# Kernel tuning notes

Hardware: AMD Instinct MI355X
Metric: run time of the kernel (lower is better)

The kernel has to match this reference:

```python
import jax, jax.numpy as jnp
import numpy as np

NUM_SEQS = 4
Q_LEN = 512          # new query tokens per sequence (chunked prefill)
SEQ_LEN = 2048       # total tokens per sequence (context + query)
NUM_Q_HEADS = 32
NUM_KV_HEADS = 8
HEAD_SIZE = 128
BLOCK_SIZE = 32
BLOCKS_PER_SEQ = SEQ_LEN // BLOCK_SIZE          # 64
NUM_BLOCKS = NUM_SEQS * BLOCKS_PER_SEQ          # 256 physical blocks


def setup_inputs() -> dict:
    key = jax.random.key(0)
    k1, k2, k3 = jax.random.split(key, 3)
    query = jax.random.normal(k1, (NUM_SEQS * Q_LEN, NUM_Q_HEADS, HEAD_SIZE), dtype=jnp.float32)
    key_cache = jax.random.normal(k2, (NUM_BLOCKS, BLOCK_SIZE, NUM_KV_HEADS, HEAD_SIZE), dtype=jnp.float32)
    value_cache = jax.random.normal(k3, (NUM_BLOCKS, BLOCK_SIZE, NUM_KV_HEADS, HEAD_SIZE), dtype=jnp.float32)
    # each sequence owns a contiguous run of physical blocks (any permutation works)
    block_tables = jnp.arange(NUM_BLOCKS, dtype=jnp.int32).reshape(NUM_SEQS, BLOCKS_PER_SEQ)
    seq_lens = jnp.full((NUM_SEQS,), SEQ_LEN, dtype=jnp.int32)
    query_start_loc = jnp.arange(NUM_SEQS + 1, dtype=jnp.int32) * Q_LEN
    return {"query": query, "key_cache": key_cache, "value_cache": value_cache,
            "block_tables": block_tables, "seq_lens": seq_lens,
            "query_start_loc": query_start_loc}


def reference(query, key_cache, value_cache, block_tables, seq_lens, query_start_loc):
    # paged/unified attention, base config: causal, GQA, no window/alibi/softcap/sinks/quant
    B, NB = block_tables.shape
    BS = key_cache.shape[1]
    total_q, Hq, D = query.shape
    Kvh = key_cache.shape[2]
    G = Hq // Kvh                       # num_queries_per_kv
    Lq = total_q // B                   # uniform query len per seq (matches query_start_loc)
    S = NB * BS                         # max kv length covered by block table
    scale = D ** -0.5

    q = query.reshape(B, Lq, Kvh, G, D)
    # gather paged KV: [B, NB, BS, Kvh, D] -> [B, S, Kvh, D]
    k = key_cache[block_tables].reshape(B, S, Kvh, D)
    v = value_cache[block_tables].reshape(B, S, Kvh, D)

    scores = jnp.einsum('blkgd,bskd->blkgs', q, k) * scale  # [B, Lq, Kvh, G, S]

    # absolute query positions: context_len + local pos, context_len = seq_len - Lq
    q_abs = (seq_lens - Lq)[:, None] + jnp.arange(Lq, dtype=seq_lens.dtype)[None, :]  # [B, Lq]
    kpos = jnp.arange(S, dtype=seq_lens.dtype)
    causal = kpos[None, None, :] <= q_abs[:, :, None]                 # key <= query pos
    valid = kpos[None, None, :] < seq_lens[:, None, None]             # key within seq
    mask = causal & valid                                             # [B, Lq, S]

    neg_inf = jnp.asarray(-jnp.inf, scores.dtype)
    scores = jnp.where(mask[:, :, None, None, :], scores, neg_inf)
    p = jax.nn.softmax(scores, axis=-1)
    out = jnp.einsum('blkgs,bskd->blkgd', p, v)                       # [B, Lq, Kvh, G, D]
    return out.reshape(total_q, Hq, D)
```

## Files before the change

kernel.cpp:

```cpp
#include <hip/hip_runtime.h>
#include <hip/hip_bf16.h>

typedef __bf16 bf16;
typedef __attribute__((ext_vector_type(8))) __bf16 bf16x8;
typedef __attribute__((ext_vector_type(4))) __bf16 bf16x4;
typedef __attribute__((ext_vector_type(4))) float f32x4;

static constexpr int NSEQ = 4;
static constexpr int LQ   = 512;
static constexpr int HQN  = 32;
static constexpr int HKVN = 8;
static constexpr int GQ   = 4;
static constexpr int DH   = 128;
static constexpr int BPS  = 64;
static constexpr int SKV  = 2048;
static constexpr int KVB  = 64;
static constexpr int QBL  = 32;
static constexpr int VST  = 72;

__device__ __forceinline__ bf16x8 cvt8(const float4& a, const float4& b) {
  bf16x8 o;
  o[0] = (bf16)a.x; o[1] = (bf16)a.y; o[2] = (bf16)a.z; o[3] = (bf16)a.w;
  o[4] = (bf16)b.x; o[5] = (bf16)b.y; o[6] = (bf16)b.z; o[7] = (bf16)b.w;
  return o;
}

__global__ void prep_k(const float* __restrict__ kc, const int* __restrict__ bt,
                       bf16* __restrict__ kb) {
  int e = (blockIdx.x * 256 + threadIdx.x) * 8;
  int d = e & 127;
  int s = (e >> 7) & 2047;
  int h = (e >> 18) & 7;
  int b = e >> 21;
  int pb = bt[b * BPS + (s >> 5)];
  const float* src = kc + (((size_t)pb * 32 + (s & 31)) * 8 + h) * 128 + d;
  float4 a = *(const float4*)src;
  float4 c = *(const float4*)(src + 4);
  *(bf16x8*)(kb + e) = cvt8(a, c);
}

__global__ void prep_vt(const float* __restrict__ vc, const int* __restrict__ bt,
                        bf16* __restrict__ vt) {
  __shared__ __align__(16) bf16 T[64][136];
  int bid = blockIdx.x;
  int st = bid & 31;
  int h  = (bid >> 5) & 7;
  int b  = bid >> 8;
  int tid = threadIdx.x;
  {
    int s  = tid >> 2;
    int d0 = (tid & 3) * 32;
    int sg = st * 64 + s;
    int pb = bt[b * BPS + (sg >> 5)];
    const float* src = vc + (((size_t)pb * 32 + (sg & 31)) * 8 + h) * 128 + d0;
#pragma unroll
    for (int k = 0; k < 4; ++k) {
      float4 a = *(const float4*)(src + 8 * k);
      float4 c = *(const float4*)(src + 8 * k + 4);
      *(bf16x8*)&T[s][d0 + 8 * k] = cvt8(a, c);
    }
  }
  __syncthreads();
  {
    int d  = tid & 127;
    int g2 = tid >> 7;
    bf16* dst = vt + (((size_t)(b * 8 + h)) * 128 + d) * SKV + st * 64 + g2 * 32;
#pragma unroll
    for (int k = 0; k < 4; ++k) {
      bf16x8 o;
#pragma unroll
      for (int j = 0; j < 8; ++j) o[j] = T[g2 * 32 + k * 8 + j][d];
      *(bf16x8*)(dst + 8 * k) = o;
    }
  }
}

template <bool WS>
__global__ __launch_bounds__(256, 2)
void attn_kern(const float* __restrict__ q, const float* __restrict__ kc,
               const float* __restrict__ vc, const int* __restrict__ bt,
               const int* __restrict__ seq_lens, const bf16* __restrict__ kb,
               const bf16* __restrict__ vtb, float* __restrict__ out) {
  __shared__ __align__(16) bf16 Kl[2][64][136];
  __shared__ __align__(16) bf16 Vl[2][128 * VST];

  int bid = (int)blockIdx.x;
  int hi  = bid >> 8;
  int u   = bid & 255;
  int xcd = u & 7;
  int k2  = u >> 3;
  int c   = (k2 >> 3) | (xcd << 2);
  int i   = k2 & 7;
  int qt  = hi ? (15 - i) : i;
  int h   = c & 7;
  int b   = c >> 3;
  int lb  = qt * QBL;

  int tid  = (int)threadIdx.x;
  int w    = tid >> 6;
  int lane = tid & 63;
  int lq   = lane & 15;
  int lg   = lane >> 4;

  int ctx = seq_lens[b] - LQ;
  int nt  = (ctx + lb + QBL + KVB - 1) / KVB;

  const float CEXP = 0.08838834764831843f * 1.44269504088896340f;
  const float TH8  = 8.0f / CEXP;

  int hq = h * GQ + w;
  bf16x8 qf[2][4];
#pragma unroll
  for (int n = 0; n < 2; ++n) {
    const float* qp = q + (((size_t)(b * LQ + lb + n * 16 + lq)) * HQN + hq) * DH + lg * 8;
#pragma unroll
    for (int kk = 0; kk < 4; ++kk) {
      float4 a = *(const float4*)(qp + kk * 32);
      float4 c2 = *(const float4*)(qp + kk * 32 + 4);
      qf[n][kk] = cvt8(a, c2);
    }
  }

  f32x4 accO[2][8];
  f32x4 zero = {0.f, 0.f, 0.f, 0.f};
#pragma unroll
  for (int m = 0; m < 2; ++m)
#pragma unroll
    for (int nd = 0; nd < 8; ++nd) accO[m][nd] = zero;
  float mrun[2] = {-1e30f, -1e30f};
  float lrun[2] = {0.f, 0.f};

  const int* btr = bt + b * BPS;
  const bf16* kbase = WS ? kb  + (size_t)(b * 8 + h) * SKV * DH : nullptr;
  const bf16* vbase = WS ? vtb + (size_t)(b * 8 + h) * DH * SKV : nullptr;

  int ks_ = tid >> 2, kd0 = (tid & 3) * 32;
  int vd_ = tid >> 1, vu  = tid & 1;
  int vxw = ((vd_ >> 3) & 3) << 1;

  bf16x8 kpre[4], vpre[4];
  auto ldKV = [&](int t) {
    const bf16* ks = kbase + ((size_t)t * 64 + ks_) * DH + kd0;
#pragma unroll
    for (int k = 0; k < 4; ++k) kpre[k] = *(const bf16x8*)(ks + 8 * k);
    const bf16* vs = vbase + (size_t)vd_ * SKV + t * 64 + vu * 32;
#pragma unroll
    for (int k = 0; k < 4; ++k) vpre[k] = *(const bf16x8*)(vs + 8 * k);
  };
  auto stKV = [&](int bb) {
#pragma unroll
    for (int k = 0; k < 4; ++k) *(bf16x8*)&Kl[bb][ks_][kd0 + 8 * k] = kpre[k];
#pragma unroll
    for (int k = 0; k < 4; ++k) {
      int g = (4 * vu + k) ^ vxw;
      *(bf16x8*)&Vl[bb][vd_ * VST + (g << 3)] = vpre[k];
    }
  };

  auto compute = [&](int t, int bb) {
    f32x4 accS[4][2];
#pragma unroll
    for (int m = 0; m < 4; ++m)
#pragma unroll
      for (int n = 0; n < 2; ++n) accS[m][n] = zero;
    __builtin_amdgcn_s_setprio(1);
#pragma unroll
    for (int m = 0; m < 4; ++m) {
      bf16x8 ak[4];
#pragma unroll
      for (int kk = 0; kk < 4; ++kk)
        ak[kk] = *(const bf16x8*)&Kl[bb][m * 16 + lq][kk * 32 + lg * 8];
#pragma unroll
      for (int n = 0; n < 2; ++n)
#pragma unroll
        for (int kk = 0; kk < 4; ++kk)
          accS[m][n] = __builtin_amdgcn_mfma_f32_16x16x32_bf16(ak[kk], qf[n][kk], accS[m][n], 0, 0, 0);
    }
    __builtin_amdgcn_s_setprio(0);

    if (t * KVB + KVB - 1 > ctx + lb) {
#pragma unroll
      for (int m = 0; m < 4; ++m) {
        int sg = t * 64 + m * 16 + lg * 4;
#pragma unroll
        for (int n = 0; n < 2; ++n) {
          int qpos = ctx + lb + n * 16 + lq;
#pragma unroll
          for (int r = 0; r < 4; ++r)
            if (sg + r > qpos) accS[m][n][r] = -1e30f;
        }
      }
    }

#pragma unroll
    for (int n = 0; n < 2; ++n) {
      float mx = accS[0][n][0];
#pragma unroll
      for (int m = 0; m < 4; ++m)
#pragma unroll
        for (int r = 0; r < 4; ++r) mx = fmaxf(mx, accS[m][n][r]);
      mx = fmaxf(mx, __shfl_xor(mx, 16));
      mx = fmaxf(mx, __shfl_xor(mx, 32));
      if (!__all(mx <= mrun[n] + TH8)) {
        float mnew = fmaxf(mrun[n], mx);
        float corr = exp2f((mrun[n] - mnew) * CEXP);
        mrun[n] = mnew;
        lrun[n] *= corr;
        float cb[4];
#pragma unroll
        for (int r = 0; r < 4; ++r) cb[r] = __shfl(corr, lg * 4 + r);
#pragma unroll
        for (int nd = 0; nd < 8; ++nd)
#pragma unroll
          for (int r = 0; r < 4; ++r) accO[n][nd][r] *= cb[r];
      }
      float psum = 0.f;
#pragma unroll
      for (int m = 0; m < 4; ++m)
#pragma unroll
        for (int r = 0; r < 4; ++r) {
          float p = exp2f((accS[m][n][r] - mrun[n]) * CEXP);
          psum += p;
          accS[m][n][r] = p;
        }
      lrun[n] += psum;
    }

    bf16x8 ap[2][2];
#pragma unroll
    for (int n = 0; n < 2; ++n)
#pragma unroll
      for (int ks3 = 0; ks3 < 2; ++ks3) {
#pragma unroll
        for (int e = 0; e < 4; ++e) {
          ap[n][ks3][e]     = (bf16)accS[2 * ks3][n][e];
          ap[n][ks3][4 + e] = (bf16)accS[2 * ks3 + 1][n][e];
        }
      }

    __builtin_amdgcn_s_setprio(1);
#pragma unroll
    for (int nd = 0; nd < 8; ++nd) {
      int d   = nd * 16 + lq;
      int vxr = ((d >> 3) & 3) << 1;
      int rb  = d * VST + 4 * (lg & 1);
#pragma unroll
      for (int ks3 = 0; ks3 < 2; ++ks3) {
        int g0 = 4 * ks3 + (lg >> 1);
        bf16x4 lo = *(const bf16x4*)&Vl[bb][rb + ((g0 ^ vxr) << 3)];
        bf16x4 hi2 = *(const bf16x4*)&Vl[bb][rb + (((g0 + 2) ^ vxr) << 3)];
        bf16x8 bv;
#pragma unroll
        for (int e = 0; e < 4; ++e) { bv[e] = lo[e]; bv[4 + e] = hi2[e]; }
#pragma unroll
        for (int n = 0; n < 2; ++n)
          accO[n][nd] = __builtin_amdgcn_mfma_f32_16x16x32_bf16(ap[n][ks3], bv, accO[n][nd], 0, 0, 0);
      }
    }
    __builtin_amdgcn_s_setprio(0);
  };

  if (WS) {
    ldKV(0);
    stKV(0);
    if (nt > 1) ldKV(1);
    __syncthreads();
    for (int t = 0; t < nt; ++t) {
      int cur = t & 1;
      if (t + 1 < nt) {
        stKV(cur ^ 1);
        if (t + 2 < nt) ldKV(t + 2);
      }
      compute(t, cur);
      __syncthreads();
    }
  } else {
    for (int t = 0; t < nt; ++t) {
      {
        int s  = tid >> 2;
        int d0 = (tid & 3) * 32;
        int pb = btr[t * 2 + (s >> 5)];
        const float* ksrc = kc + (((size_t)pb * 32 + (s & 31)) * 8 + h) * 128 + d0;
#pragma unroll
        for (int k = 0; k < 4; ++k) {
          float4 a = *(const float4*)(ksrc + 8 * k);
          float4 c2 = *(const float4*)(ksrc + 8 * k + 4);
          *(bf16x8*)&Kl[0][s][d0 + 8 * k] = cvt8(a, c2);
        }
        int d  = tid & 127;
        int sh = tid >> 7;
        int vxf = ((d >> 3) & 3) << 1;
        int pbv = btr[t * 2 + sh];
        const float* vsrc = vc + (((size_t)pbv * 32) * 8 + h) * 128 + d;
#pragma unroll
        for (int k = 0; k < 8; ++k) {
          bf16x4 o;
#pragma unroll
          for (int j = 0; j < 4; ++j) o[j] = (bf16)vsrc[(size_t)(k * 4 + j) * 1024];
          int g = (4 * sh + (k >> 1)) ^ vxf;
          *(bf16x4*)&Vl[0][d * VST + (g << 3) + 4 * (k & 1)] = o;
        }
      }
      __syncthreads();
      compute(t, 0);
      __syncthreads();
    }
  }

#pragma unroll
  for (int n = 0; n < 2; ++n) {
    lrun[n] += __shfl_xor(lrun[n], 16);
    lrun[n] += __shfl_xor(lrun[n], 32);
    lrun[n] = 1.f / lrun[n];
  }
#pragma unroll
  for (int m2 = 0; m2 < 2; ++m2) {
    float rb[4];
#pragma unroll
    for (int r = 0; r < 4; ++r) rb[r] = __shfl(lrun[m2], lg * 4 + r);
#pragma unroll
    for (int r = 0; r < 4; ++r) {
      float* op = out + (((size_t)(b * LQ + lb + m2 * 16 + lg * 4 + r)) * HQN + hq) * DH + lq;
#pragma unroll
      for (int nd = 0; nd < 8; ++nd) op[nd * 16] = accO[m2][nd][r] * rb[r];
    }
  }
}

extern "C" void kernel_launch(void* const* d_in, const int* in_sizes, int n_in,
                              void* d_out, int out_size, void* d_ws, size_t ws_size,
                              hipStream_t stream) {
  const float* q  = (const float*)d_in[0];
  const float* kc = (const float*)d_in[1];
  const float* vc = (const float*)d_in[2];
  const int* bt   = (const int*)d_in[3];
  const int* sl   = (const int*)d_in[4];
  float* out = (float*)d_out;

  size_t half = (size_t)NSEQ * HKVN * SKV * DH;
  size_t need = 2 * half * sizeof(bf16);
  if (ws_size >= need) {
    bf16* kb = (bf16*)d_ws;
    bf16* vt = kb + half;
    hipLaunchKernelGGL(prep_k, dim3(4096), dim3(256), 0, stream, kc, bt, kb);
    hipLaunchKernelGGL(prep_vt, dim3(1024), dim3(256), 0, stream, vc, bt, vt);
    hipLaunchKernelGGL((attn_kern<true>), dim3(512), dim3(256), 0, stream,
                       q, kc, vc, bt, sl, kb, vt, out);
  } else {
    hipLaunchKernelGGL((attn_kern<false>), dim3(512), dim3(256), 0, stream,
                       q, kc, vc, bt, sl, (const bf16*)nullptr, (const bf16*)nullptr, out);
  }
}
```

Baseline: 116.6 us.

## Load V fragments directly from global memory into registers, dropping LDS staging

```diff
diff --git a/kernel.cpp b/kernel.cpp
--- a/kernel.cpp
+++ b/kernel.cpp
@@ -16,7 +16,6 @@
 static constexpr int SKV  = 2048;
 static constexpr int KVB  = 64;
 static constexpr int QBL  = 32;
-static constexpr int VST  = 72;
 
 __device__ __forceinline__ bf16x8 cvt8(const float4& a, const float4& b) {
   bf16x8 o;
@@ -82,7 +81,6 @@
                const int* __restrict__ seq_lens, const bf16* __restrict__ kb,
                const bf16* __restrict__ vtb, float* __restrict__ out) {
   __shared__ __align__(16) bf16 Kl[2][64][136];
-  __shared__ __align__(16) bf16 Vl[2][128 * VST];
 
   int bid = (int)blockIdx.x;
   int hi  = bid >> 8;
@@ -135,29 +133,47 @@
   const bf16* vbase = WS ? vtb + (size_t)(b * 8 + h) * DH * SKV : nullptr;
 
   int ks_ = tid >> 2, kd0 = (tid & 3) * 32;
-  int vd_ = tid >> 1, vu  = tid & 1;
-  int vxw = ((vd_ >> 3) & 3) << 1;
-
-  bf16x8 kpre[4], vpre[4];
-  auto ldKV = [&](int t) {
+
+  bf16x8 kpre[4];
+  auto ldK = [&](int t) {
     const bf16* ks = kbase + ((size_t)t * 64 + ks_) * DH + kd0;
 #pragma unroll
     for (int k = 0; k < 4; ++k) kpre[k] = *(const bf16x8*)(ks + 8 * k);
-    const bf16* vs = vbase + (size_t)vd_ * SKV + t * 64 + vu * 32;
-#pragma unroll
-    for (int k = 0; k < 4; ++k) vpre[k] = *(const bf16x8*)(vs + 8 * k);
   };
-  auto stKV = [&](int bb) {
+  auto stK = [&](int bb) {
 #pragma unroll
     for (int k = 0; k < 4; ++k) *(bf16x8*)&Kl[bb][ks_][kd0 + 8 * k] = kpre[k];
-#pragma unroll
-    for (int k = 0; k < 4; ++k) {
-      int g = (4 * vu + k) ^ vxw;
-      *(bf16x8*)&Vl[bb][vd_ * VST + (g << 3)] = vpre[k];
-    }
   };
 
+  int vcol = (lg >> 1) * 8 + (lg & 1) * 4;
+
   auto compute = [&](int t, int bb) {
+    bf16x4 vlo[8][2], vhi[8][2];
+    if (WS) {
+#pragma unroll
+      for (int nd = 0; nd < 8; ++nd) {
+        const bf16* vp = vbase + (size_t)(nd * 16 + lq) * SKV + t * 64 + vcol;
+#pragma unroll
+        for (int ks3 = 0; ks3 < 2; ++ks3) {
+          vlo[nd][ks3] = *(const bf16x4*)(vp + ks3 * 32);
+          vhi[nd][ks3] = *(const bf16x4*)(vp + ks3 * 32 + 16);
+        }
+      }
+    } else {
+#pragma unroll
+      for (int nd = 0; nd < 8; ++nd)
+#pragma unroll
+        for (int ks3 = 0; ks3 < 2; ++ks3)
+#pragma unroll
+          for (int e = 0; e < 4; ++e) {
+            int s0 = t * 64 + ks3 * 32 + vcol + e;
+            int s1 = s0 + 16;
+            int pb0 = btr[s0 >> 5], pb1 = btr[s1 >> 5];
+            vlo[nd][ks3][e] = (bf16)vc[(((size_t)pb0 * 32 + (s0 & 31)) * 8 + h) * 128 + nd * 16 + lq];
+            vhi[nd][ks3][e] = (bf16)vc[(((size_t)pb1 * 32 + (s1 & 31)) * 8 + h) * 128 + nd * 16 + lq];
+          }
+    }
+
     f32x4 accS[4][2];
 #pragma unroll
     for (int m = 0; m < 4; ++m)
@@ -241,17 +257,14 @@
     __builtin_amdgcn_s_setprio(1);
 #pragma unroll
     for (int nd = 0; nd < 8; ++nd) {
-      int d   = nd * 16 + lq;
-      int vxr = ((d >> 3) & 3) << 1;
-      int rb  = d * VST + 4 * (lg & 1);
 #pragma unroll
       for (int ks3 = 0; ks3 < 2; ++ks3) {
-        int g0 = 4 * ks3 + (lg >> 1);
-        bf16x4 lo = *(const bf16x4*)&Vl[bb][rb + ((g0 ^ vxr) << 3)];
-        bf16x4 hi2 = *(const bf16x4*)&Vl[bb][rb + (((g0 + 2) ^ vxr) << 3)];
         bf16x8 bv;
 #pragma unroll
-        for (int e = 0; e < 4; ++e) { bv[e] = lo[e]; bv[4 + e] = hi2[e]; }
+        for (int e = 0; e < 4; ++e) {
+          bv[e]     = vlo[nd][ks3][e];
+          bv[4 + e] = vhi[nd][ks3][e];
+        }
 #pragma unroll
         for (int n = 0; n < 2; ++n)
           accO[n][nd] = __builtin_amdgcn_mfma_f32_16x16x32_bf16(ap[n][ks3], bv, accO[n][nd], 0, 0, 0);
@@ -261,15 +274,15 @@
   };
 
   if (WS) {
-    ldKV(0);
-    stKV(0);
-    if (nt > 1) ldKV(1);
+    ldK(0);
+    stK(0);
+    if (nt > 1) ldK(1);
     __syncthreads();
     for (int t = 0; t < nt; ++t) {
       int cur = t & 1;
       if (t + 1 < nt) {
-        stKV(cur ^ 1);
-        if (t + 2 < nt) ldKV(t + 2);
+        stK(cur ^ 1);
+        if (t + 2 < nt) ldK(t + 2);
       }
       compute(t, cur);
       __syncthreads();
@@ -286,19 +299,6 @@
           float4 a = *(const float4*)(ksrc + 8 * k);
           float4 c2 = *(const float4*)(ksrc + 8 * k + 4);
           *(bf16x8*)&Kl[0][s][d0 + 8 * k] = cvt8(a, c2);
-        }
-        int d  = tid & 127;
-        int sh = tid >> 7;
-        int vxf = ((d >> 3) & 3) << 1;
-        int pbv = btr[t * 2 + sh];
-        const float* vsrc = vc + (((size_t)pbv * 32) * 8 + h) * 128 + d;
-#pragma unroll
-        for (int k = 0; k < 8; ++k) {
-          bf16x4 o;
-#pragma unroll
-          for (int j = 0; j < 4; ++j) o[j] = (bf16)vsrc[(size_t)(k * 4 + j) * 1024];
-          int g = (4 * sh + (k >> 1)) ^ vxf;
-          *(bf16x4*)&Vl[0][d * VST + (g << 3) + 4 * (k & 1)] = o;
         }
       }
       __syncthreads();
```

New measurement: 258.5 us. 2.22x slower.

## Split attention work across 8 waves per block, one 16-row query tile each

Applied to the files above, without the earlier changes.

```diff
diff --git a/kernel.cpp b/kernel.cpp
--- a/kernel.cpp
+++ b/kernel.cpp
@@ -75,12 +75,10 @@
   }
 }
 
-template <bool WS>
-__global__ __launch_bounds__(256, 2)
-void attn_kern(const float* __restrict__ q, const float* __restrict__ kc,
-               const float* __restrict__ vc, const int* __restrict__ bt,
-               const int* __restrict__ seq_lens, const bf16* __restrict__ kb,
-               const bf16* __restrict__ vtb, float* __restrict__ out) {
+__global__ __launch_bounds__(512, 2)
+void attn_ns(const float* __restrict__ q, const int* __restrict__ seq_lens,
+             const bf16* __restrict__ kb, const bf16* __restrict__ vtb,
+             float* __restrict__ out) {
   __shared__ __align__(16) bf16 Kl[2][64][136];
   __shared__ __align__(16) bf16 Vl[2][128 * VST];
 
@@ -98,6 +96,199 @@
 
   int tid  = (int)threadIdx.x;
   int w    = tid >> 6;
+  int g    = w & 3;
+  int nh   = w >> 2;
+  int lane = tid & 63;
+  int lq   = lane & 15;
+  int lg   = lane >> 4;
+
+  int ctx = seq_lens[b] - LQ;
+  int nt  = (ctx + lb + QBL + KVB - 1) / KVB;
+  int qpos = ctx + lb + nh * 16 + lq;
+
+  const float CEXP = 0.08838834764831843f * 1.44269504088896340f;
+  const float TH8  = 8.0f / CEXP;
+
+  int hq = h * GQ + g;
+  bf16x8 qf[4];
+  {
+    const float* qp = q + (((size_t)(b * LQ + lb + nh * 16 + lq)) * HQN + hq) * DH + lg * 8;
+#pragma unroll
+    for (int kk = 0; kk < 4; ++kk) {
+      float4 a = *(const float4*)(qp + kk * 32);
+      float4 c2 = *(const float4*)(qp + kk * 32 + 4);
+      qf[kk] = cvt8(a, c2);
+    }
+  }
+
+  f32x4 accO[8];
+  f32x4 zero = {0.f, 0.f, 0.f, 0.f};
+#pragma unroll
+  for (int nd = 0; nd < 8; ++nd) accO[nd] = zero;
+  float mrun = -1e30f, lrun = 0.f;
+
+  const bf16* kbase = kb  + (size_t)(b * 8 + h) * SKV * DH;
+  const bf16* vbase = vtb + (size_t)(b * 8 + h) * DH * SKV;
+
+  int ks_ = tid >> 3, kd0 = (tid & 7) * 16;
+  int vd_ = tid >> 2, vq  = tid & 3;
+  int vxw = ((vd_ >> 3) & 3) << 1;
+
+  bf16x8 kpre[2], vpre[2];
+  auto ldKV = [&](int t) {
+    const bf16* ks = kbase + ((size_t)t * 64 + ks_) * DH + kd0;
+    kpre[0] = *(const bf16x8*)ks;
+    kpre[1] = *(const bf16x8*)(ks + 8);
+    const bf16* vs = vbase + (size_t)vd_ * SKV + t * 64 + vq * 16;
+    vpre[0] = *(const bf16x8*)vs;
+    vpre[1] = *(const bf16x8*)(vs + 8);
+  };
+  auto stKV = [&](int bb) {
+    *(bf16x8*)&Kl[bb][ks_][kd0]     = kpre[0];
+    *(bf16x8*)&Kl[bb][ks_][kd0 + 8] = kpre[1];
+#pragma unroll
+    for (int k = 0; k < 2; ++k) {
+      int gg = (2 * vq + k) ^ vxw;
+      *(bf16x8*)&Vl[bb][vd_ * VST + (gg << 3)] = vpre[k];
+    }
+  };
+
+  auto compute = [&](int t, int bb) {
+    f32x4 accS[4];
+#pragma unroll
+    for (int m = 0; m < 4; ++m) accS[m] = zero;
+    __builtin_amdgcn_s_setprio(1);
+#pragma unroll
+    for (int m = 0; m < 4; ++m) {
+#pragma unroll
+      for (int kk = 0; kk < 4; ++kk) {
+        bf16x8 ak = *(const bf16x8*)&Kl[bb][m * 16 + lq][kk * 32 + lg * 8];
+        accS[m] = __builtin_amdgcn_mfma_f32_16x16x32_bf16(ak, qf[kk], accS[m], 0, 0, 0);
+      }
+    }
+    __builtin_amdgcn_s_setprio(0);
+
+    if (t * KVB + KVB - 1 > ctx + lb) {
+#pragma unroll
+      for (int m = 0; m < 4; ++m) {
+        int sg = t * 64 + m * 16 + lg * 4;
+#pragma unroll
+        for (int r = 0; r < 4; ++r)
+          if (sg + r > qpos) accS[m][r] = -1e30f;
+      }
+    }
+
+    {
+      float mx = accS[0][0];
+#pragma unroll
+      for (int m = 0; m < 4; ++m)
+#pragma unroll
+        for (int r = 0; r < 4; ++r) mx = fmaxf(mx, accS[m][r]);
+      mx = fmaxf(mx, __shfl_xor(mx, 16));
+      mx = fmaxf(mx, __shfl_xor(mx, 32));
+      if (!__all(mx <= mrun + TH8)) {
+        float mnew = fmaxf(mrun, mx);
+        float corr = exp2f((mrun - mnew) * CEXP);
+        mrun = mnew;
+        lrun *= corr;
+        float cb[4];
+#pragma unroll
+        for (int r = 0; r < 4; ++r) cb[r] = __shfl(corr, lg * 4 + r);
+#pragma unroll
+        for (int nd = 0; nd < 8; ++nd)
+#pragma unroll
+          for (int r = 0; r < 4; ++r) accO[nd][r] *= cb[r];
+      }
+      float ps[4] = {0.f, 0.f, 0.f, 0.f};
+#pragma unroll
+      for (int m = 0; m < 4; ++m)
+#pragma unroll
+        for (int r = 0; r < 4; ++r) {
+          float p = exp2f((accS[m][r] - mrun) * CEXP);
+          ps[r] += p;
+          accS[m][r] = p;
+        }
+      lrun += (ps[0] + ps[1]) + (ps[2] + ps[3]);
+    }
+
+    bf16x8 ap[2];
+#pragma unroll
+    for (int ks3 = 0; ks3 < 2; ++ks3)
+#pragma unroll
+      for (int e = 0; e < 4; ++e) {
+        ap[ks3][e]     = (bf16)accS[2 * ks3][e];
+        ap[ks3][4 + e] = (bf16)accS[2 * ks3 + 1][e];
+      }
+
+    __builtin_amdgcn_s_setprio(1);
+#pragma unroll
+    for (int nd = 0; nd < 8; ++nd) {
+      int d   = nd * 16 + lq;
+      int vxr = ((d >> 3) & 3) << 1;
+      int rb  = d * VST + 4 * (lg & 1);
+#pragma unroll
+      for (int ks3 = 0; ks3 < 2; ++ks3) {
+        int g0 = 4 * ks3 + (lg >> 1);
+        bf16x4 lo  = *(const bf16x4*)&Vl[bb][rb + ((g0 ^ vxr) << 3)];
+        bf16x4 hi2 = *(const bf16x4*)&Vl[bb][rb + (((g0 + 2) ^ vxr) << 3)];
+        bf16x8 bv;
+#pragma unroll
+        for (int e = 0; e < 4; ++e) { bv[e] = lo[e]; bv[4 + e] = hi2[e]; }
+        accO[nd] = __builtin_amdgcn_mfma_f32_16x16x32_bf16(ap[ks3], bv, accO[nd], 0, 0, 0);
+      }
+    }
+    __builtin_amdgcn_s_setprio(0);
+  };
+
+  ldKV(0);
+  stKV(0);
+  if (nt > 1) ldKV(1);
+  __syncthreads();
+  for (int t = 0; t < nt; ++t) {
+    int cur = t & 1;
+    if (t + 1 < nt) {
+      stKV(cur ^ 1);
+      if (t + 2 < nt) ldKV(t + 2);
+    }
+    compute(t, cur);
+    __syncthreads();
+  }
+
+  lrun += __shfl_xor(lrun, 16);
+  lrun += __shfl_xor(lrun, 32);
+  float linv = 1.f / lrun;
+  float rb[4];
+#pragma unroll
+  for (int r = 0; r < 4; ++r) rb[r] = __shfl(linv, lg * 4 + r);
+#pragma unroll
+  for (int r = 0; r < 4; ++r) {
+    float* op = out + (((size_t)(b * LQ + lb + nh * 16 + lg * 4 + r)) * HQN + hq) * DH + lq;
+#pragma unroll
+    for (int nd = 0; nd < 8; ++nd) op[nd * 16] = accO[nd][r] * rb[r];
+  }
+}
+
+__global__ __launch_bounds__(256, 2)
+void attn_fb(const float* __restrict__ q, const float* __restrict__ kc,
+             const float* __restrict__ vc, const int* __restrict__ bt,
+             const int* __restrict__ seq_lens, float* __restrict__ out) {
+  __shared__ __align__(16) bf16 Kl[64][136];
+  __shared__ __align__(16) bf16 Vl[128 * VST];
+
+  int bid = (int)blockIdx.x;
+  int hi  = bid >> 8;
+  int u   = bid & 255;
+  int xcd = u & 7;
+  int k2  = u >> 3;
+  int c   = (k2 >> 3) | (xcd << 2);
+  int i   = k2 & 7;
+  int qt  = hi ? (15 - i) : i;
+  int h   = c & 7;
+  int b   = c >> 3;
+  int lb  = qt * QBL;
+
+  int tid  = (int)threadIdx.x;
+  int w    = tid >> 6;
   int lane = tid & 63;
   int lq   = lane & 15;
   int lg   = lane >> 4;
@@ -131,52 +322,52 @@
   float lrun[2] = {0.f, 0.f};
 
   const int* btr = bt + b * BPS;
-  const bf16* kbase = WS ? kb  + (size_t)(b * 8 + h) * SKV * DH : nullptr;
-  const bf16* vbase = WS ? vtb + (size_t)(b * 8 + h) * DH * SKV : nullptr;
-
-  int ks_ = tid >> 2, kd0 = (tid & 3) * 32;
-  int vd_ = tid >> 1, vu  = tid & 1;
-  int vxw = ((vd_ >> 3) & 3) << 1;
-
-  bf16x8 kpre[4], vpre[4];
-  auto ldKV = [&](int t) {
-    const bf16* ks = kbase + ((size_t)t * 64 + ks_) * DH + kd0;
-#pragma unroll
-    for (int k = 0; k < 4; ++k) kpre[k] = *(const bf16x8*)(ks + 8 * k);
-    const bf16* vs = vbase + (size_t)vd_ * SKV + t * 64 + vu * 32;
-#pragma unroll
-    for (int k = 0; k < 4; ++k) vpre[k] = *(const bf16x8*)(vs + 8 * k);
-  };
-  auto stKV = [&](int bb) {
-#pragma unroll
-    for (int k = 0; k < 4; ++k) *(bf16x8*)&Kl[bb][ks_][kd0 + 8 * k] = kpre[k];
-#pragma unroll
-    for (int k = 0; k < 4; ++k) {
-      int g = (4 * vu + k) ^ vxw;
-      *(bf16x8*)&Vl[bb][vd_ * VST + (g << 3)] = vpre[k];
-    }
-  };
-
-  auto compute = [&](int t, int bb) {
+
+  for (int t = 0; t < nt; ++t) {
+    {
+      int s  = tid >> 2;
+      int d0 = (tid & 3) * 32;
+      int pb = btr[t * 2 + (s >> 5)];
+      const float* ksrc = kc + (((size_t)pb * 32 + (s & 31)) * 8 + h) * 128 + d0;
+#pragma unroll
+      for (int k = 0; k < 4; ++k) {
+        float4 a = *(const float4*)(ksrc + 8 * k);
+        float4 c2 = *(const float4*)(ksrc + 8 * k + 4);
+        *(bf16x8*)&Kl[s][d0 + 8 * k] = cvt8(a, c2);
+      }
+      int d  = tid & 127;
+      int sh = tid >> 7;
+      int vxf = ((d >> 3) & 3) << 1;
+      int pbv = btr[t * 2 + sh];
+      const float* vsrc = vc + (((size_t)pbv * 32) * 8 + h) * 128 + d;
+#pragma unroll
+      for (int k = 0; k < 8; ++k) {
+        bf16x4 o;
+#pragma unroll
+        for (int j = 0; j < 4; ++j) o[j] = (bf16)vsrc[(size_t)(k * 4 + j) * 1024];
+        int gg = (4 * sh + (k >> 1)) ^ vxf;
+        *(bf16x4*)&Vl[d * VST + (gg << 3) + 4 * (k & 1)] = o;
+      }
+    }
+    __syncthreads();
+
     f32x4 accS[4][2];
 #pragma unroll
     for (int m = 0; m < 4; ++m)
 #pragma unroll
       for (int n = 0; n < 2; ++n) accS[m][n] = zero;
-    __builtin_amdgcn_s_setprio(1);
 #pragma unroll
     for (int m = 0; m < 4; ++m) {
       bf16x8 ak[4];
 #pragma unroll
       for (int kk = 0; kk < 4; ++kk)
-        ak[kk] = *(const bf16x8*)&Kl[bb][m * 16 + lq][kk * 32 + lg * 8];
+        ak[kk] = *(const bf16x8*)&Kl[m * 16 + lq][kk * 32 + lg * 8];
 #pragma unroll
       for (int n = 0; n < 2; ++n)
 #pragma unroll
         for (int kk = 0; kk < 4; ++kk)
           accS[m][n] = __builtin_amdgcn_mfma_f32_16x16x32_bf16(ak[kk], qf[n][kk], accS[m][n], 0, 0, 0);
     }
-    __builtin_amdgcn_s_setprio(0);
 
     if (t * KVB + KVB - 1 > ctx + lb) {
 #pragma unroll
@@ -230,15 +421,13 @@
 #pragma unroll
     for (int n = 0; n < 2; ++n)
 #pragma unroll
-      for (int ks3 = 0; ks3 < 2; ++ks3) {
+      for (int ks3 = 0; ks3 < 2; ++ks3)
 #pragma unroll
         for (int e = 0; e < 4; ++e) {
           ap[n][ks3][e]     = (bf16)accS[2 * ks3][n][e];
           ap[n][ks3][4 + e] = (bf16)accS[2 * ks3 + 1][n][e];
         }
-      }
-
-    __builtin_amdgcn_s_setprio(1);
+
 #pragma unroll
     for (int nd = 0; nd < 8; ++nd) {
       int d   = nd * 16 + lq;
@@ -247,8 +436,8 @@
 #pragma unroll
       for (int ks3 = 0; ks3 < 2; ++ks3) {
         int g0 = 4 * ks3 + (lg >> 1);
-        bf16x4 lo = *(const bf16x4*)&Vl[bb][rb + ((g0 ^ vxr) << 3)];
-        bf16x4 hi2 = *(const bf16x4*)&Vl[bb][rb + (((g0 + 2) ^ vxr) << 3)];
+        bf16x4 lo  = *(const bf16x4*)&Vl[rb + ((g0 ^ vxr) << 3)];
+        bf16x4 hi2 = *(const bf16x4*)&Vl[rb + (((g0 + 2) ^ vxr) << 3)];
         bf16x8 bv;
 #pragma unroll
         for (int e = 0; e < 4; ++e) { bv[e] = lo[e]; bv[4 + e] = hi2[e]; }
@@ -257,54 +446,7 @@
           accO[n][nd] = __builtin_amdgcn_mfma_f32_16x16x32_bf16(ap[n][ks3], bv, accO[n][nd], 0, 0, 0);
       }
     }
-    __builtin_amdgcn_s_setprio(0);
-  };
-
-  if (WS) {
-    ldKV(0);
-    stKV(0);
-    if (nt > 1) ldKV(1);
     __syncthreads();
-    for (int t = 0; t < nt; ++t) {
-      int cur = t & 1;
-      if (t + 1 < nt) {
-        stKV(cur ^ 1);
-        if (t + 2 < nt) ldKV(t + 2);
-      }
-      compute(t, cur);
-      __syncthreads();
-    }
-  } else {
-    for (int t = 0; t < nt; ++t) {
-      {
-        int s  = tid >> 2;
-        int d0 = (tid & 3) * 32;
-        int pb = btr[t * 2 + (s >> 5)];
-        const float* ksrc = kc + (((size_t)pb * 32 + (s & 31)) * 8 + h) * 128 + d0;
-#pragma unroll
-        for (int k = 0; k < 4; ++k) {
-          float4 a = *(const float4*)(ksrc + 8 * k);
-          float4 c2 = *(const float4*)(ksrc + 8 * k + 4);
-          *(bf16x8*)&Kl[0][s][d0 + 8 * k] = cvt8(a, c2);
-        }
-        int d  = tid & 127;
-        int sh = tid >> 7;
-        int vxf = ((d >> 3) & 3) << 1;
-        int pbv = btr[t * 2 + sh];
-        const float* vsrc = vc + (((size_t)pbv * 32) * 8 + h) * 128 + d;
-#pragma unroll
-        for (int k = 0; k < 8; ++k) {
-          bf16x4 o;
-#pragma unroll
-          for (int j = 0; j < 4; ++j) o[j] = (bf16)vsrc[(size_t)(k * 4 + j) * 1024];
-          int g = (4 * sh + (k >> 1)) ^ vxf;
-          *(bf16x4*)&Vl[0][d * VST + (g << 3) + 4 * (k & 1)] = o;
-        }
-      }
-      __syncthreads();
-      compute(t, 0);
-      __syncthreads();
-    }
   }
 
 #pragma unroll
@@ -344,10 +486,9 @@
     bf16* vt = kb + half;
     hipLaunchKernelGGL(prep_k, dim3(4096), dim3(256), 0, stream, kc, bt, kb);
     hipLaunchKernelGGL(prep_vt, dim3(1024), dim3(256), 0, stream, vc, bt, vt);
-    hipLaunchKernelGGL((attn_kern<true>), dim3(512), dim3(256), 0, stream,
-                       q, kc, vc, bt, sl, kb, vt, out);
+    hipLaunchKernelGGL(attn_ns, dim3(512), dim3(512), 0, stream, q, sl, kb, vt, out);
   } else {
-    hipLaunchKernelGGL((attn_kern<false>), dim3(512), dim3(256), 0, stream,
-                       q, kc, vc, bt, sl, (const bf16*)nullptr, (const bf16*)nullptr, out);
-  }
-}
+    hipLaunchKernelGGL(attn_fb, dim3(512), dim3(256), 0, stream,
+                       q, kc, vc, bt, sl, out);
+  }
+}
```

New measurement: 148.5 us. 27.3% more time.
